# Kernel optimization log

Hardware: AMD Instinct MI355X
Metric: run time of the kernel (lower is better)

The kernel has to match this reference:

```python
import jax, jax.numpy as jnp
import numpy as np

D_MODEL = 1024
N_HEADS = 16
HEAD_DIM = D_MODEL // N_HEADS
B, S = 2, 2048


def setup_inputs() -> dict:
    key = jax.random.key(0)
    k1, k2, k3, k4, k5 = jax.random.split(key, 5)
    scale = 1.0 / np.sqrt(D_MODEL)
    return {
        "x": jax.random.normal(k1, (B, S, D_MODEL), dtype=jnp.float32),
        "mask": jnp.ones((B, S), dtype=jnp.int32),
        "W_qkv": jax.random.normal(k2, (D_MODEL, 3 * D_MODEL), dtype=jnp.float32) * scale,
        "b_qkv": jnp.zeros((3 * D_MODEL,), dtype=jnp.float32),
        "W_proj": jax.random.normal(k3, (D_MODEL, D_MODEL), dtype=jnp.float32) * scale,
        "b_proj": jnp.zeros((D_MODEL,), dtype=jnp.float32),
    }


def reference(x, mask, W_qkv, b_qkv, W_proj, b_proj):
    b, s, d = x.shape
    qkv = x @ W_qkv + b_qkv                                  # [B,S,3D]
    qkv = qkv.reshape(b, s, 3, N_HEADS, HEAD_DIM)
    qkv = jnp.transpose(qkv, (2, 0, 3, 1, 4))                # [3,B,H,S,Dh]
    q, k, v = qkv[0], qkv[1], qkv[2]
    scores = jnp.einsum("bhqd,bhkd->bhqk", q, k) / np.sqrt(HEAD_DIM)
    if mask is not None:
        m = mask[:, None, None, :]                           # [B,1,1,S]
        scores = jnp.where(m == 0, -jnp.inf, scores)
    attn = jax.nn.softmax(scores, axis=-1)
    out = jnp.einsum("bhqk,bhkd->bhqd", attn, v)             # [B,H,S,Dh]
    out = jnp.transpose(out, (0, 2, 1, 3)).reshape(b, s, d)  # [B,S,D]
    return out @ W_proj + b_proj
```

## Files before the change

### kernel.cpp

```cpp
#include <hip/hip_runtime.h>

typedef unsigned short u16;
typedef unsigned int u32;
typedef __bf16 bf16x8 __attribute__((ext_vector_type(8)));
typedef float f32x4 __attribute__((ext_vector_type(4)));
typedef float f32x16 __attribute__((ext_vector_type(16)));

#define D_MODEL 1024
#define SQ 2048
#define NH 16
#define HD 64
#define KVB 128
#define NT (SQ / KVB)
#define QSCALE 0.1803368801111204f

__device__ __forceinline__ u16 f2bf(float f) {
    u32 u = __builtin_bit_cast(u32, f);
    u = (u + 0x7fffu + ((u >> 16) & 1u)) >> 16;
    return (u16)u;
}

__device__ __forceinline__ f32x4 mfma16(bf16x8 a, bf16x8 b, f32x4 c) {
    return __builtin_amdgcn_mfma_f32_16x16x32_bf16(a, b, c, 0, 0, 0);
}
__device__ __forceinline__ f32x16 mfma32(bf16x8 a, bf16x8 b, f32x16 c) {
    return __builtin_amdgcn_mfma_f32_32x32x16_bf16(a, b, c, 0, 0, 0);
}

__device__ __forceinline__ bf16x8 ld16(const void* p) {
    return __builtin_bit_cast(bf16x8, *(const int4*)p);
}

__device__ __forceinline__ void gl_lds16(const u16* g, u16* l) {
    __builtin_amdgcn_global_load_lds((const __attribute__((address_space(1))) unsigned int*)g,
                                     (__attribute__((address_space(3))) unsigned int*)l, 16, 0, 0);
}

__device__ __forceinline__ u32 cvtpk(float a, float b) {
    u32 r;
    asm("v_cvt_pk_bf16_f32 %0, %1, %2" : "=v"(r) : "v"(a), "v"(b));
    return r;
}

__device__ __forceinline__ void swap32(u32& a, u32& b) {
    asm("v_permlane32_swap_b32 %0, %1" : "+v"(a), "+v"(b));
}


__global__ __launch_bounds__(256) void cvt_f32_bf16(const float* __restrict__ in,
                                                    u16* __restrict__ out, int n4) {
    int i = blockIdx.x * blockDim.x + threadIdx.x;
    if (i >= n4) return;
    float4 v = ((const float4*)in)[i];
    ushort4 o;
    o.x = f2bf(v.x); o.y = f2bf(v.y); o.z = f2bf(v.z); o.w = f2bf(v.w);
    ((ushort4*)out)[i] = o;
}

__global__ __launch_bounds__(256) void tconv(const float* __restrict__ in,
                                             u16* __restrict__ out, int K, int N) {
    __shared__ float t[32][33];
    const int n0 = blockIdx.x * 32, k0 = blockIdx.y * 32;
    const int tx = threadIdx.x, ty = threadIdx.y;
#pragma unroll
    for (int i = 0; i < 4; ++i)
        t[ty + 8 * i][tx] = in[(size_t)(k0 + ty + 8 * i) * N + n0 + tx];
    __syncthreads();
#pragma unroll
    for (int i = 0; i < 4; ++i)
        out[(size_t)(n0 + ty + 8 * i) * K + k0 + tx] = f2bf(t[tx][ty + 8 * i]);
}

__global__ __launch_bounds__(256) void vtrans(const u16* __restrict__ Vw, u16* __restrict__ Vtw) {
    __shared__ u16 T[64][72];
    const int bh = blockIdx.y, s0 = blockIdx.x * 64, tid = threadIdx.x;
    const int r = tid >> 3, cb = tid & 7;
#pragma unroll
    for (int i = 0; i < 2; ++i) {
        int rr = r + 32 * i;
        int4 v = *(const int4*)(Vw + ((size_t)bh * SQ + s0 + rr) * HD + cb * 8);
        *(int4*)&T[rr][cb * 8] = v;
    }
    __syncthreads();
#pragma unroll
    for (int i = 0; i < 2; ++i) {
        int d = r + 32 * i, so = cb * 8;
        u16 tmp[8];
#pragma unroll
        for (int j = 0; j < 8; ++j) tmp[j] = T[so + j][d];
        *(int4*)(Vtw + ((size_t)bh * HD + d) * SQ + s0 + so) = *(int4*)tmp;
    }
}


template <int MODE>
__global__ __launch_bounds__(256) void gemm128(const u16* __restrict__ A,
                                               const u16* __restrict__ Bt,
                                               const float* __restrict__ bias,
                                               u16* __restrict__ Qw, u16* __restrict__ Kw,
                                               u16* __restrict__ Vw, float* __restrict__ Out) {
    __shared__ u16 As[128 * 32];
    __shared__ u16 Bs[128 * 32];

    const int tid = threadIdx.x;
    const int l = tid & 63, w = tid >> 6;
    const int l16 = l & 15, lq = l >> 4;
    const int wm = w >> 1, wn = w & 1;
    const int m0 = blockIdx.y * 128, n0 = blockIdx.x * 128;

    f32x4 acc[4][4];
#pragma unroll
    for (int i = 0; i < 4; ++i)
#pragma unroll
        for (int j = 0; j < 4; ++j) acc[i][j] = f32x4{0.f, 0.f, 0.f, 0.f};

    const int srow = 32 * w + (l >> 2);
    const u16* aSrc = A + (size_t)(m0 + srow) * 1024 + (l & 3) * 8;
    const u16* bSrc = Bt + (size_t)(n0 + srow) * 1024 + (l & 3) * 8;
    u16* AsW = As + w * 1024;
    u16* BsW = Bs + w * 1024;

    for (int kt = 0; kt < 32; ++kt) {
        __syncthreads();
        gl_lds16(aSrc + kt * 32, AsW);
        gl_lds16(aSrc + kt * 32 + (size_t)16 * 1024, AsW + 512);
        gl_lds16(bSrc + kt * 32, BsW);
        gl_lds16(bSrc + kt * 32 + (size_t)16 * 1024, BsW + 512);
        __syncthreads();

        bf16x8 af[4], bfr[4];
#pragma unroll
        for (int mi = 0; mi < 4; ++mi)
            af[mi] = ld16((char*)As + (wm * 64 + mi * 16 + l16) * 64 + lq * 16);
#pragma unroll
        for (int ni = 0; ni < 4; ++ni)
            bfr[ni] = ld16((char*)Bs + (wn * 64 + ni * 16 + l16) * 64 + lq * 16);
#pragma unroll
        for (int mi = 0; mi < 4; ++mi)
#pragma unroll
            for (int ni = 0; ni < 4; ++ni)
                acc[mi][ni] = mfma16(af[mi], bfr[ni], acc[mi][ni]);
    }

#pragma unroll
    for (int mi = 0; mi < 4; ++mi) {
#pragma unroll
        for (int ni = 0; ni < 4; ++ni) {
            const int n = n0 + wn * 64 + ni * 16 + l16;
            const float bv = bias[n];
#pragma unroll
            for (int r = 0; r < 4; ++r) {
                const int m = m0 + wm * 64 + mi * 16 + 4 * lq + r;
                float v = acc[mi][ni][r] + bv;
                if (MODE == 0) {
                    const int which = n >> 10;
                    const int h = (n >> 6) & 15;
                    const int d = n & 63;
                    const int b = m >> 11, s = m & 2047;
                    const size_t bh = (size_t)(b * NH + h);
                    if (which == 0)
                        Qw[(bh * SQ + s) * HD + d] = f2bf(v * QSCALE);
                    else if (which == 1)
                        Kw[(bh * SQ + s) * HD + d] = f2bf(v);
                    else
                        Vw[(bh * SQ + s) * HD + d] = f2bf(v);
                } else {
                    Out[(size_t)m * 1024 + n] = v;
                }
            }
        }
    }
}


__global__ __launch_bounds__(256) void gemm_proj(const u16* __restrict__ A,
                                                 const u16* __restrict__ Bt,
                                                 const float* __restrict__ bias,
                                                 float* __restrict__ Out) {
    __shared__ u16 As[128 * 32];
    __shared__ u16 Bs[64 * 32];

    const int tid = threadIdx.x;
    const int l = tid & 63, w = tid >> 6;
    const int l16 = l & 15, lq = l >> 4;
    const int wm = w >> 1, wn = w & 1;
    const int m0 = blockIdx.y * 128, n0 = blockIdx.x * 64;

    f32x4 acc[4][2];
#pragma unroll
    for (int i = 0; i < 4; ++i)
#pragma unroll
        for (int j = 0; j < 2; ++j) acc[i][j] = f32x4{0.f, 0.f, 0.f, 0.f};

    const int srowA = 32 * w + (l >> 2);
    const int srowB = 16 * w + (l >> 2);
    const u16* aSrc = A + (size_t)(m0 + srowA) * 1024 + (l & 3) * 8;
    const u16* bSrc = Bt + (size_t)(n0 + srowB) * 1024 + (l & 3) * 8;
    u16* AsW = As + w * 1024;
    u16* BsW = Bs + w * 512;

    for (int kt = 0; kt < 32; ++kt) {
        __syncthreads();
        gl_lds16(aSrc + kt * 32, AsW);
        gl_lds16(aSrc + kt * 32 + (size_t)16 * 1024, AsW + 512);
        gl_lds16(bSrc + kt * 32, BsW);
        __syncthreads();

        bf16x8 af[4], bfr[2];
#pragma unroll
        for (int mi = 0; mi < 4; ++mi)
            af[mi] = ld16((char*)As + (wm * 64 + mi * 16 + l16) * 64 + lq * 16);
#pragma unroll
        for (int ni = 0; ni < 2; ++ni)
            bfr[ni] = ld16((char*)Bs + (wn * 32 + ni * 16 + l16) * 64 + lq * 16);
#pragma unroll
        for (int mi = 0; mi < 4; ++mi)
#pragma unroll
            for (int ni = 0; ni < 2; ++ni)
                acc[mi][ni] = mfma16(af[mi], bfr[ni], acc[mi][ni]);
    }

#pragma unroll
    for (int mi = 0; mi < 4; ++mi) {
#pragma unroll
        for (int ni = 0; ni < 2; ++ni) {
            const int n = n0 + wn * 32 + ni * 16 + l16;
            const float bv = bias[n];
#pragma unroll
            for (int r = 0; r < 4; ++r) {
                const int m = m0 + wm * 64 + mi * 16 + 4 * lq + r;
                Out[(size_t)m * 1024 + n] = acc[mi][ni][r] + bv;
            }
        }
    }
}


__global__ __launch_bounds__(256) void attn128(const u16* __restrict__ Qw, const u16* __restrict__ Kw,
                                               const u16* __restrict__ Vtw, const int* __restrict__ mask,
                                               u16* __restrict__ Ow) {
    __shared__ u16 Ks[2][KVB * HD];
    __shared__ u16 Vs[2][HD * KVB];
    __shared__ float smaddL[SQ];
    __shared__ int allFlag;

    const int tid = threadIdx.x;
    const int l = tid & 63, w = tid >> 6;
    const int q = l & 31, hl = l >> 5;
    const int bh = blockIdx.y, b = bh >> 4, h = bh & 15;
    const int q0 = blockIdx.x * 128;

    if (tid == 0) allFlag = 1;
    __syncthreads();
    {
        const int4* m4 = (const int4*)(mask + (size_t)b * SQ) + tid * 2;
        int4 a0 = m4[0], a1 = m4[1];
        int ok = a0.x && a0.y && a0.z && a0.w && a1.x && a1.y && a1.z && a1.w;
        float* sp = &smaddL[tid * 8];
        sp[0] = a0.x ? 0.f : -1e30f; sp[1] = a0.y ? 0.f : -1e30f;
        sp[2] = a0.z ? 0.f : -1e30f; sp[3] = a0.w ? 0.f : -1e30f;
        sp[4] = a1.x ? 0.f : -1e30f; sp[5] = a1.y ? 0.f : -1e30f;
        sp[6] = a1.z ? 0.f : -1e30f; sp[7] = a1.w ? 0.f : -1e30f;
        if (!ok) allFlag = 0;
    }

    bf16x8 aq[4];
    {
        const u16* qb = Qw + ((size_t)bh * SQ + q0 + w * 32 + q) * HD + hl * 8;
#pragma unroll
        for (int kc = 0; kc < 4; ++kc) aq[kc] = ld16(qb + kc * 16);
    }

    const int cok = ((l & 7) ^ (l >> 3)) * 8;
    const u16* kbase = Kw + ((size_t)bh * SQ + 32 * w + (l >> 3)) * HD + cok;
    const int cov0 = ((l & 15) ^ (l >> 4)) * 8;
    const int cov1 = cov0 ^ 32;
    const u16* vbase = Vtw + ((size_t)bh * HD + 16 * w + (l >> 4)) * SQ;

    __syncthreads();
    const bool anyMasked = (allFlag == 0);

    {
        u16* kd = (u16*)Ks[0] + 32 * w * HD;
        u16* vd = (u16*)Vs[0] + 16 * w * KVB;
#pragma unroll
        for (int j = 0; j < 4; ++j) {
            gl_lds16(kbase + j * 8 * HD, kd + j * 8 * HD);
            gl_lds16(vbase + j * 4 * SQ + ((j & 1) ? cov1 : cov0), vd + j * 4 * KVB);
        }
    }
    __syncthreads();

    f32x16 accO[2];
#pragma unroll
    for (int r = 0; r < 16; ++r) { accO[0][r] = 0.f; accO[1][r] = 0.f; }
    float ssum = 0.f;

    const int swzq = (q & 7) << 4;
    const int hb = hl * 16;

    int p = 0;
    for (int kt = 0; kt < NT; ++kt) {
        if (kt + 1 < NT) {
            u16* kdn = (u16*)Ks[p ^ 1] + 32 * w * HD;
            u16* vdn = (u16*)Vs[p ^ 1] + 16 * w * KVB;
            const u16* ks = kbase + (size_t)(kt + 1) * KVB * HD;
            const u16* vs = vbase + (kt + 1) * KVB;
#pragma unroll
            for (int j = 0; j < 4; ++j) {
                gl_lds16(ks + j * 8 * HD, kdn + j * 8 * HD);
                gl_lds16(vs + j * 4 * SQ + ((j & 1) ? cov1 : cov0), vdn + j * 4 * KVB);
            }
        }

        const char* Ksp = (const char*)Ks[p];
        const char* Vsp = (const char*)Vs[p];

        f32x16 s[4];
        if (anyMasked) {
#pragma unroll
            for (int kb = 0; kb < 4; ++kb)
#pragma unroll
                for (int q2 = 0; q2 < 4; ++q2) {
                    float4 mv = *(const float4*)&smaddL[kt * KVB + 32 * kb + 8 * q2 + 4 * hl];
                    s[kb][4 * q2 + 0] = mv.x; s[kb][4 * q2 + 1] = mv.y;
                    s[kb][4 * q2 + 2] = mv.z; s[kb][4 * q2 + 3] = mv.w;
                }
        } else {
#pragma unroll
            for (int kb = 0; kb < 4; ++kb)
#pragma unroll
                for (int r = 0; r < 16; ++r) s[kb][r] = 0.f;
        }

        __builtin_amdgcn_s_setprio(1);
#pragma unroll
        for (int kb = 0; kb < 4; ++kb) {
            const int krow = 32 * kb + q;
#pragma unroll
            for (int kc = 0; kc < 4; ++kc) {
                bf16x8 kf = ld16(Ksp + krow * 128 + ((kc * 32 + hb) ^ swzq));
                s[kb] = mfma32(kf, aq[kc], s[kb]);
            }
        }
        __builtin_amdgcn_s_setprio(0);

        u32 pw[4][4][2];
        float r0 = 0.f, r1 = 0.f, r2 = 0.f, r3 = 0.f;
#pragma unroll
        for (int kb = 0; kb < 4; ++kb)
#pragma unroll
            for (int q2 = 0; q2 < 4; ++q2) {
                float p0 = __builtin_amdgcn_exp2f(s[kb][4 * q2 + 0]);
                float p1 = __builtin_amdgcn_exp2f(s[kb][4 * q2 + 1]);
                float p2 = __builtin_amdgcn_exp2f(s[kb][4 * q2 + 2]);
                float p3 = __builtin_amdgcn_exp2f(s[kb][4 * q2 + 3]);
                r0 += p0; r1 += p1; r2 += p2; r3 += p3;
                pw[kb][q2][0] = cvtpk(p0, p1);
                pw[kb][q2][1] = cvtpk(p2, p3);
            }
        float rs = (r0 + r1) + (r2 + r3);
        rs += __shfl_xor(rs, 32);
        ssum += rs;

        bf16x8 pf[8];
#pragma unroll
        for (int kb = 0; kb < 4; ++kb)
#pragma unroll
            for (int c1 = 0; c1 < 2; ++c1) {
                u32 x0 = pw[kb][2 * c1][0], y0 = pw[kb][2 * c1 + 1][0];
                u32 x1 = pw[kb][2 * c1][1], y1 = pw[kb][2 * c1 + 1][1];
                swap32(x0, y0);
                swap32(x1, y1);
                int4 f;
                f.x = x0; f.y = x1; f.z = y0; f.w = y1;
                pf[2 * kb + c1] = __builtin_bit_cast(bf16x8, f);
            }

        __builtin_amdgcn_s_setprio(1);
#pragma unroll
        for (int db = 0; db < 2; ++db) {
            const int vrow = 32 * db + q;
#pragma unroll
            for (int kc = 0; kc < 8; ++kc) {
                bf16x8 vf = ld16(Vsp + vrow * 256 + ((kc * 32 + hb) ^ swzq));
                accO[db] = mfma32(vf, pf[kc], accO[db]);
            }
        }
        __builtin_amdgcn_s_setprio(0);

        __syncthreads();
        p ^= 1;
    }

    const float inv = ssum > 0.f ? 1.f / ssum : 0.f;
    u16* ot = (u16*)Ks + w * 2048;
#pragma unroll
    for (int db = 0; db < 2; ++db)
#pragma unroll
        for (int m = 0; m < 4; ++m) {
            u32 w0 = cvtpk(accO[db][4 * m + 0] * inv, accO[db][4 * m + 1] * inv);
            u32 w1 = cvtpk(accO[db][4 * m + 2] * inv, accO[db][4 * m + 3] * inv);
            const int dbase = 32 * db + 8 * m + 4 * hl;
            uint2 pr; pr.x = w0; pr.y = w1;
            *(uint2*)((char*)ot + q * 128 + ((dbase * 2) ^ ((q & 7) << 4))) = pr;
        }
    __syncthreads();
#pragma unroll
    for (int i = 0; i < 4; ++i) {
        const int qr = 8 * i + (l >> 3);
        int4 vv = *(const int4*)((char*)ot + qr * 128 + (((l & 7) * 16) ^ ((qr & 7) << 4)));
        *(int4*)(Ow + ((size_t)b * SQ + q0 + 32 * w + qr) * D_MODEL + h * HD + (l & 7) * 8) = vv;
    }
}


extern "C" void kernel_launch(void* const* d_in, const int* in_sizes, int n_in,
                              void* d_out, int out_size, void* d_ws, size_t ws_size,
                              hipStream_t stream) {
    (void)in_sizes; (void)n_in; (void)out_size; (void)ws_size;
    const float* x = (const float*)d_in[0];
    const int* mask = (const int*)d_in[1];
    const float* Wqkv = (const float*)d_in[2];
    const float* bqkv = (const float*)d_in[3];
    const float* Wproj = (const float*)d_in[4];
    const float* bproj = (const float*)d_in[5];
    float* out = (float*)d_out;

    char* ws = (char*)d_ws;
    const size_t MB = 1024 * 1024;
    u16* x_bf = (u16*)(ws);
    u16* wq_t = (u16*)(ws + 8 * MB);
    u16* wp_t = (u16*)(ws + 14 * MB);
    u16* Qw   = (u16*)(ws + 16 * MB);
    u16* Kw   = (u16*)(ws + 24 * MB);
    u16* Vtw  = (u16*)(ws + 32 * MB);
    u16* Ow   = (u16*)(ws + 40 * MB);
    u16* Vw   = (u16*)(ws + 40 * MB);

    cvt_f32_bf16<<<4096, 256, 0, stream>>>(x, x_bf, 4096 * 1024 / 4);
    tconv<<<dim3(96, 32), dim3(32, 8), 0, stream>>>(Wqkv, wq_t, 1024, 3072);
    tconv<<<dim3(32, 32), dim3(32, 8), 0, stream>>>(Wproj, wp_t, 1024, 1024);
    gemm128<0><<<dim3(24, 32), 256, 0, stream>>>(x_bf, wq_t, bqkv, Qw, Kw, Vw, nullptr);
    vtrans<<<dim3(32, 32), 256, 0, stream>>>(Vw, Vtw);
    attn128<<<dim3(16, 32), 256, 0, stream>>>(Qw, Kw, Vtw, mask, Ow);
    gemm_proj<<<dim3(16, 32), 256, 0, stream>>>(Ow, wp_t, bproj, out);
}
```

Before: 203.1 us.

## Split attention KV tiles across warp pairs with 64-query blocks and reduce partials

The attention kernel now processes 64 queries per block, with four warps split into two query halves and two key halves that each handle 32 keys of every 64-key tile. At the end, the partial outputs and row sums are combined through shared memory. The grid doubles to 1024 blocks, LDS per block shrinks (64-key tiles, bf16 mask), and launch bounds request 4 blocks per SM. The aim is better occupancy and latency hiding, at the cost of an extra cross-warp reduction and more barrier steps per key.

```diff
diff --git a/kernel.cpp b/kernel.cpp
--- a/kernel.cpp
+++ b/kernel.cpp
@@ -10,8 +10,6 @@
 #define SQ 2048
 #define NH 16
 #define HD 64
-#define KVB 128
-#define NT (SQ / KVB)
 #define QSCALE 0.1803368801111204f
 
 __device__ __forceinline__ u16 f2bf(float f) {
@@ -236,19 +234,20 @@
 }
 
 
-__global__ __launch_bounds__(256) void attn128(const u16* __restrict__ Qw, const u16* __restrict__ Kw,
-                                               const u16* __restrict__ Vtw, const int* __restrict__ mask,
-                                               u16* __restrict__ Ow) {
-    __shared__ u16 Ks[2][KVB * HD];
-    __shared__ u16 Vs[2][HD * KVB];
-    __shared__ float smaddL[SQ];
+__global__ __launch_bounds__(256, 4) void attn64(const u16* __restrict__ Qw, const u16* __restrict__ Kw,
+                                                 const u16* __restrict__ Vtw, const int* __restrict__ mask,
+                                                 u16* __restrict__ Ow) {
+    __shared__ u16 Ks[2][64 * 64];
+    __shared__ u16 Vs[2][64 * 64];
+    __shared__ u16 smadd16[SQ];
     __shared__ int allFlag;
 
     const int tid = threadIdx.x;
     const int l = tid & 63, w = tid >> 6;
     const int q = l & 31, hl = l >> 5;
+    const int qh = w & 1, kb = w >> 1;
     const int bh = blockIdx.y, b = bh >> 4, h = bh & 15;
-    const int q0 = blockIdx.x * 128;
+    const int q0 = blockIdx.x * 64;
 
     if (tid == 0) allFlag = 1;
     __syncthreads();
@@ -256,37 +255,36 @@
         const int4* m4 = (const int4*)(mask + (size_t)b * SQ) + tid * 2;
         int4 a0 = m4[0], a1 = m4[1];
         int ok = a0.x && a0.y && a0.z && a0.w && a1.x && a1.y && a1.z && a1.w;
-        float* sp = &smaddL[tid * 8];
-        sp[0] = a0.x ? 0.f : -1e30f; sp[1] = a0.y ? 0.f : -1e30f;
-        sp[2] = a0.z ? 0.f : -1e30f; sp[3] = a0.w ? 0.f : -1e30f;
-        sp[4] = a1.x ? 0.f : -1e30f; sp[5] = a1.y ? 0.f : -1e30f;
-        sp[6] = a1.z ? 0.f : -1e30f; sp[7] = a1.w ? 0.f : -1e30f;
+        const u16 NEG = f2bf(-1e30f);
+        u16* sp = &smadd16[tid * 8];
+        sp[0] = a0.x ? (u16)0 : NEG; sp[1] = a0.y ? (u16)0 : NEG;
+        sp[2] = a0.z ? (u16)0 : NEG; sp[3] = a0.w ? (u16)0 : NEG;
+        sp[4] = a1.x ? (u16)0 : NEG; sp[5] = a1.y ? (u16)0 : NEG;
+        sp[6] = a1.z ? (u16)0 : NEG; sp[7] = a1.w ? (u16)0 : NEG;
         if (!ok) allFlag = 0;
     }
 
     bf16x8 aq[4];
     {
-        const u16* qb = Qw + ((size_t)bh * SQ + q0 + w * 32 + q) * HD + hl * 8;
+        const u16* qb = Qw + ((size_t)bh * SQ + q0 + qh * 32 + q) * HD + hl * 8;
 #pragma unroll
         for (int kc = 0; kc < 4; ++kc) aq[kc] = ld16(qb + kc * 16);
     }
 
-    const int cok = ((l & 7) ^ (l >> 3)) * 8;
-    const u16* kbase = Kw + ((size_t)bh * SQ + 32 * w + (l >> 3)) * HD + cok;
-    const int cov0 = ((l & 15) ^ (l >> 4)) * 8;
-    const int cov1 = cov0 ^ 32;
-    const u16* vbase = Vtw + ((size_t)bh * HD + 16 * w + (l >> 4)) * SQ;
+    const int srow = l >> 3, scb = (l & 7) ^ srow;
+    const u16* kbase = Kw + ((size_t)bh * SQ + 16 * w + srow) * HD + scb * 8;
+    const u16* vbase = Vtw + ((size_t)bh * HD + 16 * w + srow) * SQ + scb * 8;
 
     __syncthreads();
     const bool anyMasked = (allFlag == 0);
 
     {
-        u16* kd = (u16*)Ks[0] + 32 * w * HD;
-        u16* vd = (u16*)Vs[0] + 16 * w * KVB;
-#pragma unroll
-        for (int j = 0; j < 4; ++j) {
-            gl_lds16(kbase + j * 8 * HD, kd + j * 8 * HD);
-            gl_lds16(vbase + j * 4 * SQ + ((j & 1) ? cov1 : cov0), vd + j * 4 * KVB);
+        u16* kd = (u16*)Ks[0] + w * 1024;
+        u16* vd = (u16*)Vs[0] + w * 1024;
+#pragma unroll
+        for (int j = 0; j < 2; ++j) {
+            gl_lds16(kbase + j * 8 * HD, kd + j * 512);
+            gl_lds16(vbase + (size_t)j * 8 * SQ, vd + j * 512);
         }
     }
     __syncthreads();
@@ -298,93 +296,82 @@
 
     const int swzq = (q & 7) << 4;
     const int hb = hl * 16;
+    const int krow = 32 * kb + q;
 
     int p = 0;
-    for (int kt = 0; kt < NT; ++kt) {
-        if (kt + 1 < NT) {
-            u16* kdn = (u16*)Ks[p ^ 1] + 32 * w * HD;
-            u16* vdn = (u16*)Vs[p ^ 1] + 16 * w * KVB;
-            const u16* ks = kbase + (size_t)(kt + 1) * KVB * HD;
-            const u16* vs = vbase + (kt + 1) * KVB;
-#pragma unroll
-            for (int j = 0; j < 4; ++j) {
-                gl_lds16(ks + j * 8 * HD, kdn + j * 8 * HD);
-                gl_lds16(vs + j * 4 * SQ + ((j & 1) ? cov1 : cov0), vdn + j * 4 * KVB);
+    for (int kt = 0; kt < SQ / 64; ++kt) {
+        if (kt + 1 < SQ / 64) {
+            u16* kd = (u16*)Ks[p ^ 1] + w * 1024;
+            u16* vd = (u16*)Vs[p ^ 1] + w * 1024;
+            const u16* ks = kbase + (size_t)(kt + 1) * 64 * HD;
+            const u16* vs = vbase + (kt + 1) * 64;
+#pragma unroll
+            for (int j = 0; j < 2; ++j) {
+                gl_lds16(ks + j * 8 * HD, kd + j * 512);
+                gl_lds16(vs + (size_t)j * 8 * SQ, vd + j * 512);
             }
         }
 
         const char* Ksp = (const char*)Ks[p];
         const char* Vsp = (const char*)Vs[p];
 
-        f32x16 s[4];
+        f32x16 s;
         if (anyMasked) {
 #pragma unroll
-            for (int kb = 0; kb < 4; ++kb)
-#pragma unroll
-                for (int q2 = 0; q2 < 4; ++q2) {
-                    float4 mv = *(const float4*)&smaddL[kt * KVB + 32 * kb + 8 * q2 + 4 * hl];
-                    s[kb][4 * q2 + 0] = mv.x; s[kb][4 * q2 + 1] = mv.y;
-                    s[kb][4 * q2 + 2] = mv.z; s[kb][4 * q2 + 3] = mv.w;
-                }
+            for (int r = 0; r < 16; ++r) {
+                int key = kt * 64 + kb * 32 + (r & 3) + 8 * (r >> 2) + 4 * hl;
+                u32 bits = (u32)smadd16[key] << 16;
+                s[r] = __builtin_bit_cast(float, bits);
+            }
         } else {
 #pragma unroll
-            for (int kb = 0; kb < 4; ++kb)
-#pragma unroll
-                for (int r = 0; r < 16; ++r) s[kb][r] = 0.f;
+            for (int r = 0; r < 16; ++r) s[r] = 0.f;
         }
 
         __builtin_amdgcn_s_setprio(1);
 #pragma unroll
-        for (int kb = 0; kb < 4; ++kb) {
-            const int krow = 32 * kb + q;
-#pragma unroll
-            for (int kc = 0; kc < 4; ++kc) {
-                bf16x8 kf = ld16(Ksp + krow * 128 + ((kc * 32 + hb) ^ swzq));
-                s[kb] = mfma32(kf, aq[kc], s[kb]);
-            }
+        for (int kc = 0; kc < 4; ++kc) {
+            bf16x8 kf = ld16(Ksp + krow * 128 + ((kc * 32 + hb) ^ swzq));
+            s = mfma32(kf, aq[kc], s);
         }
         __builtin_amdgcn_s_setprio(0);
 
-        u32 pw[4][4][2];
+        u32 pw[4][2];
         float r0 = 0.f, r1 = 0.f, r2 = 0.f, r3 = 0.f;
 #pragma unroll
-        for (int kb = 0; kb < 4; ++kb)
-#pragma unroll
-            for (int q2 = 0; q2 < 4; ++q2) {
-                float p0 = __builtin_amdgcn_exp2f(s[kb][4 * q2 + 0]);
-                float p1 = __builtin_amdgcn_exp2f(s[kb][4 * q2 + 1]);
-                float p2 = __builtin_amdgcn_exp2f(s[kb][4 * q2 + 2]);
-                float p3 = __builtin_amdgcn_exp2f(s[kb][4 * q2 + 3]);
-                r0 += p0; r1 += p1; r2 += p2; r3 += p3;
-                pw[kb][q2][0] = cvtpk(p0, p1);
-                pw[kb][q2][1] = cvtpk(p2, p3);
-            }
+        for (int q2 = 0; q2 < 4; ++q2) {
+            float p0 = __builtin_amdgcn_exp2f(s[4 * q2 + 0]);
+            float p1 = __builtin_amdgcn_exp2f(s[4 * q2 + 1]);
+            float p2 = __builtin_amdgcn_exp2f(s[4 * q2 + 2]);
+            float p3 = __builtin_amdgcn_exp2f(s[4 * q2 + 3]);
+            r0 += p0; r1 += p1; r2 += p2; r3 += p3;
+            pw[q2][0] = cvtpk(p0, p1);
+            pw[q2][1] = cvtpk(p2, p3);
+        }
         float rs = (r0 + r1) + (r2 + r3);
         rs += __shfl_xor(rs, 32);
         ssum += rs;
 
-        bf16x8 pf[8];
-#pragma unroll
-        for (int kb = 0; kb < 4; ++kb)
-#pragma unroll
-            for (int c1 = 0; c1 < 2; ++c1) {
-                u32 x0 = pw[kb][2 * c1][0], y0 = pw[kb][2 * c1 + 1][0];
-                u32 x1 = pw[kb][2 * c1][1], y1 = pw[kb][2 * c1 + 1][1];
-                swap32(x0, y0);
-                swap32(x1, y1);
-                int4 f;
-                f.x = x0; f.y = x1; f.z = y0; f.w = y1;
-                pf[2 * kb + c1] = __builtin_bit_cast(bf16x8, f);
-            }
+        bf16x8 pf[2];
+#pragma unroll
+        for (int c = 0; c < 2; ++c) {
+            u32 x0 = pw[2 * c][0], y0 = pw[2 * c + 1][0];
+            u32 x1 = pw[2 * c][1], y1 = pw[2 * c + 1][1];
+            swap32(x0, y0);
+            swap32(x1, y1);
+            int4 f;
+            f.x = x0; f.y = x1; f.z = y0; f.w = y1;
+            pf[c] = __builtin_bit_cast(bf16x8, f);
+        }
 
         __builtin_amdgcn_s_setprio(1);
 #pragma unroll
         for (int db = 0; db < 2; ++db) {
             const int vrow = 32 * db + q;
 #pragma unroll
-            for (int kc = 0; kc < 8; ++kc) {
-                bf16x8 vf = ld16(Vsp + vrow * 256 + ((kc * 32 + hb) ^ swzq));
-                accO[db] = mfma32(vf, pf[kc], accO[db]);
+            for (int c = 0; c < 2; ++c) {
+                bf16x8 vf = ld16(Vsp + vrow * 128 + ((kb * 64 + c * 32 + hb) ^ swzq));
+                accO[db] = mfma32(vf, pf[c], accO[db]);
             }
         }
         __builtin_amdgcn_s_setprio(0);
@@ -393,24 +380,47 @@
         p ^= 1;
     }
 
-    const float inv = ssum > 0.f ? 1.f / ssum : 0.f;
-    u16* ot = (u16*)Ks + w * 2048;
-#pragma unroll
-    for (int db = 0; db < 2; ++db)
-#pragma unroll
-        for (int m = 0; m < 4; ++m) {
-            u32 w0 = cvtpk(accO[db][4 * m + 0] * inv, accO[db][4 * m + 1] * inv);
-            u32 w1 = cvtpk(accO[db][4 * m + 2] * inv, accO[db][4 * m + 3] * inv);
-            const int dbase = 32 * db + 8 * m + 4 * hl;
-            uint2 pr; pr.x = w0; pr.y = w1;
-            *(uint2*)((char*)ot + q * 128 + ((dbase * 2) ^ ((q & 7) << 4))) = pr;
-        }
-    __syncthreads();
-#pragma unroll
-    for (int i = 0; i < 4; ++i) {
-        const int qr = 8 * i + (l >> 3);
-        int4 vv = *(const int4*)((char*)ot + qr * 128 + (((l & 7) * 16) ^ ((qr & 7) << 4)));
-        *(int4*)(Ow + ((size_t)b * SQ + q0 + 32 * w + qr) * D_MODEL + h * HD + (l & 7) * 8) = vv;
+    if (w >= 2) {
+        float* ssx = (float*)Vs;
+        ssx[qh * 64 + l] = ssum;
+        int4* ex = (int4*)Ks + qh * 512 + l;
+#pragma unroll
+        for (int ch = 0; ch < 8; ++ch) {
+            f32x4 qd;
+#pragma unroll
+            for (int t = 0; t < 4; ++t) qd[t] = accO[ch >> 2][(ch & 3) * 4 + t];
+            ex[ch * 64] = __builtin_bit_cast(int4, qd);
+        }
+    }
+    __syncthreads();
+    if (w < 2) {
+        const float stot = ssum + ((const float*)Vs)[w * 64 + l];
+        const float inv = stot > 0.f ? 1.f / stot : 0.f;
+        const int4* ex = (const int4*)Ks + w * 512 + l;
+#pragma unroll
+        for (int ch = 0; ch < 8; ++ch) {
+            f32x4 a = __builtin_bit_cast(f32x4, ex[ch * 64]);
+#pragma unroll
+            for (int t = 0; t < 4; ++t) accO[ch >> 2][(ch & 3) * 4 + t] += a[t];
+        }
+
+        u16* ot = (u16*)Vs + 512 + w * 2048;
+#pragma unroll
+        for (int db = 0; db < 2; ++db)
+#pragma unroll
+            for (int m = 0; m < 4; ++m) {
+                u32 w0 = cvtpk(accO[db][4 * m + 0] * inv, accO[db][4 * m + 1] * inv);
+                u32 w1 = cvtpk(accO[db][4 * m + 2] * inv, accO[db][4 * m + 3] * inv);
+                const int dbase = 32 * db + 8 * m + 4 * hl;
+                uint2 pr; pr.x = w0; pr.y = w1;
+                *(uint2*)((char*)ot + q * 128 + ((dbase * 2) ^ ((q & 7) << 4))) = pr;
+            }
+#pragma unroll
+        for (int i = 0; i < 4; ++i) {
+            const int qr = 8 * i + (l >> 3);
+            int4 vv = *(const int4*)((char*)ot + qr * 128 + (((l & 7) * 16) ^ ((qr & 7) << 4)));
+            *(int4*)(Ow + ((size_t)b * SQ + q0 + 32 * w + qr) * D_MODEL + h * HD + (l & 7) * 8) = vv;
+        }
     }
 }
 
@@ -443,6 +453,6 @@
     tconv<<<dim3(32, 32), dim3(32, 8), 0, stream>>>(Wproj, wp_t, 1024, 1024);
     gemm128<0><<<dim3(24, 32), 256, 0, stream>>>(x_bf, wq_t, bqkv, Qw, Kw, Vw, nullptr);
     vtrans<<<dim3(32, 32), 256, 0, stream>>>(Vw, Vtw);
-    attn128<<<dim3(16, 32), 256, 0, stream>>>(Qw, Kw, Vtw, mask, Ow);
+    attn64<<<dim3(32, 32), 256, 0, stream>>>(Qw, Kw, Vtw, mask, Ow);
     gemm_proj<<<dim3(16, 32), 256, 0, stream>>>(Ow, wp_t, bproj, out);
 }
```

After: 202.6 us. About the same (-0.3%).
